# Kernel tuning notes

Measured on AMD Instinct MI355X. Metric: run time of the kernel, lower is better.

The kernel has to match this reference:

```python
import jax, jax.numpy as jnp
import numpy as np

B, S, D, T = 64, 512, 768, 9  # batch, seq_len, bert hidden, tag_size


def setup_inputs() -> dict:
    key = jax.random.key(0)
    ks = jax.random.split(key, 7)
    return {
        "embeds": jax.random.normal(ks[0], (B, S, D), jnp.float32),          # frozen BERT output
        "weight": jax.random.normal(ks[1], (T, D), jnp.float32) * 0.02,      # nn.Linear(768, tag_size)
        "bias": jnp.zeros((T,), jnp.float32),
        "start_transitions": jax.random.normal(ks[2], (T,), jnp.float32) * 0.1,
        "end_transitions": jax.random.normal(ks[3], (T,), jnp.float32) * 0.1,
        "transitions": jax.random.normal(ks[4], (T, T), jnp.float32) * 0.1,
        "tags": jax.random.randint(ks[5], (B, S), 0, T),
        "mask": jnp.ones((B, S), bool),  # torchcrf requires mask[:, 0] all on
    }


def reference(embeds, weight, bias, start_transitions, end_transitions, transitions, tags, mask):
    # Linear emission head (dropout is identity at eval)
    emissions = jnp.einsum("bsd,td->bst", embeds, weight) + bias  # [B,S,T]
    maskf = mask.astype(emissions.dtype)

    # --- numerator: score of gold path (torchcrf _compute_score) ---
    emit = jnp.take_along_axis(emissions, tags[:, :, None], axis=2)[:, :, 0]  # [B,S]
    trans = transitions[tags[:, :-1], tags[:, 1:]]                            # [B,S-1]
    num = start_transitions[tags[:, 0]] + emit[:, 0]
    num = num + jnp.sum((trans + emit[:, 1:]) * maskf[:, 1:], axis=1)
    seq_ends = jnp.sum(mask.astype(jnp.int32), axis=1) - 1                    # [B]
    last_tags = jnp.take_along_axis(tags, seq_ends[:, None], axis=1)[:, 0]
    num = num + end_transitions[last_tags]

    # --- denominator: forward algorithm (torchcrf _compute_normalizer) ---
    def step(score, xs):
        e_t, m_t = xs  # [B,T], [B]
        nxt = jax.nn.logsumexp(score[:, :, None] + transitions[None] + e_t[:, None, :], axis=1)
        return jnp.where(m_t[:, None], nxt, score), None

    score0 = start_transitions[None, :] + emissions[:, 0]                     # [B,T]
    xs = (jnp.swapaxes(emissions[:, 1:], 0, 1), jnp.swapaxes(mask[:, 1:], 0, 1))
    score, _ = jax.lax.scan(step, score0, xs)
    den = jax.nn.logsumexp(score + end_transitions[None, :], axis=1)          # [B]

    llh = num - den
    return -jnp.mean(llh)  # reduction='mean', negated
```

## Files before the change

### kernel.cpp

```cpp
#include <hip/hip_runtime.h>

#define BB 64
#define SS 512
#define DD 768
#define TT 9
#define CC 64
#define LL 8

template <int CTRL>
__device__ __forceinline__ float dpp_radd(float v) {
  return v + __int_as_float(__builtin_amdgcn_update_dpp(
                 0, __float_as_int(v), CTRL, 0xF, 0xF, true));
}
__device__ __forceinline__ float wave_sum_dpp(float v) {
  v = dpp_radd<0x111>(v);
  v = dpp_radd<0x112>(v);
  v = dpp_radd<0x114>(v);
  v = dpp_radd<0x118>(v);
  v = dpp_radd<0x142>(v);
  v = dpp_radd<0x143>(v);
  return v;
}

__global__ __launch_bounds__(256) void emis_kernel(
    const float* __restrict__ embeds, const float* __restrict__ weight,
    const float* __restrict__ bias, float* __restrict__ emis) {
  const int lane  = threadIdx.x & 63;
  const int wave  = blockIdx.x * (blockDim.x >> 6) + (threadIdx.x >> 6);
  const int nwav  = gridDim.x * (blockDim.x >> 6);

  float w[TT][12];
#pragma unroll
  for (int t = 0; t < TT; ++t) {
#pragma unroll
    for (int k = 0; k < 3; ++k) {
      const float4 v = *(const float4*)(weight + t * DD + k * 256 + lane * 4);
      w[t][k * 4 + 0] = v.x; w[t][k * 4 + 1] = v.y;
      w[t][k * 4 + 2] = v.z; w[t][k * 4 + 3] = v.w;
    }
  }
  float bb[TT];
#pragma unroll
  for (int t = 0; t < TT; ++t) bb[t] = bias[t];

  for (int row = wave; row < BB * SS; row += nwav) {
    const float* ep = embeds + (size_t)row * DD;
    float e[12];
#pragma unroll
    for (int k = 0; k < 3; ++k) {
      const float4 v = *(const float4*)(ep + k * 256 + lane * 4);
      e[k * 4 + 0] = v.x; e[k * 4 + 1] = v.y;
      e[k * 4 + 2] = v.z; e[k * 4 + 3] = v.w;
    }
    float acc[TT];
#pragma unroll
    for (int t = 0; t < TT; ++t) {
      float a = 0.f;
#pragma unroll
      for (int kk = 0; kk < 12; ++kk) a = fmaf(e[kk], w[t][kk], a);
      acc[t] = wave_sum_dpp(a);
    }
    if (lane == 63) {
#pragma unroll
      for (int t = 0; t < TT; ++t)
        emis[(size_t)row * TT + t] = acc[t] + bb[t];
    }
  }
}

__global__ __launch_bounds__(64) void crf_chunk_kernel(
    const float* __restrict__ emis, const float* __restrict__ trans,
    const float* __restrict__ startt, float* __restrict__ colM) {
  const int t = blockIdx.x * 64 + threadIdx.x;
  const int b = t / (CC * TT);
  const int r = t % (CC * TT);
  const int c = r / TT;
  const int j = r % TT;

  float et[TT][TT];
#pragma unroll
  for (int i = 0; i < TT; ++i)
#pragma unroll
    for (int k = 0; k < TT; ++k)
      et[i][k] = __expf(trans[i * TT + k]);

  float e[LL * TT];
  const float* eb = emis + (size_t)(b * SS + c * LL) * TT;
#pragma unroll
  for (int q = 0; q < (LL * TT) / 4; ++q) {
    const float4 v = *(const float4*)(eb + q * 4);
    e[q * 4 + 0] = v.x; e[q * 4 + 1] = v.y;
    e[q * 4 + 2] = v.z; e[q * 4 + 3] = v.w;
  }

  float v[TT];
#pragma unroll
  for (int i = 0; i < TT; ++i) v[i] = trans[i * TT + j] + e[(LL - 1) * TT + j];

#pragma unroll
  for (int ss = LL - 2; ss >= 0; --ss) {
    float w[TT];
#pragma unroll
    for (int k = 0; k < TT; ++k) w[k] = e[ss * TT + k] + v[k];
    if (ss == 0 && c == 0) {
#pragma unroll
      for (int k = 0; k < TT; ++k) w[k] += startt[k];
      float m = w[0];
#pragma unroll
      for (int k = 1; k < TT; ++k) m = fmaxf(m, w[k]);
      float sum = 0.f;
#pragma unroll
      for (int k = 0; k < TT; ++k) sum += __expf(w[k] - m);
      const float val = m + __logf(sum);
#pragma unroll
      for (int i = 0; i < TT; ++i) v[i] = val;
    } else {
      float m = w[0];
#pragma unroll
      for (int k = 1; k < TT; ++k) m = fmaxf(m, w[k]);
      float p[TT];
#pragma unroll
      for (int k = 0; k < TT; ++k) p[k] = __expf(w[k] - m);
#pragma unroll
      for (int i = 0; i < TT; ++i) {
        float sum = 0.f;
#pragma unroll
        for (int k = 0; k < TT; ++k) sum = fmaf(et[i][k], p[k], sum);
        v[i] = m + __logf(sum);
      }
    }
  }
  float* out = colM + ((size_t)(b * CC + c) * TT + j) * TT;
#pragma unroll
  for (int i = 0; i < TT; ++i) out[i] = v[i];
}

__global__ __launch_bounds__(576) void crf_combine_kernel(
    const float* __restrict__ colM, const float* __restrict__ emis,
    const float* __restrict__ trans, const float* __restrict__ startt,
    const float* __restrict__ endt, const int* __restrict__ tags,
    float* __restrict__ partial) {
  const int b   = blockIdx.x;
  const int tid = threadIdx.x;
  __shared__ float A[CC * 81];
  __shared__ float Bm[(CC / 2) * 81];
  __shared__ float red2[16];

  const float4* src4 = (const float4*)(colM + (size_t)b * CC * 81);
  float4* A4 = (float4*)A;
  for (int q = tid; q < (CC * 81) / 4; q += 576) A4[q] = src4[q];

  const float* E  = emis + (size_t)b * SS * TT;
  const int*   tg = tags + (size_t)b * SS;
  float nsum = 0.f;
  if (tid < SS) {
    const int tt = tg[tid];
    nsum = E[tid * TT + tt];
    nsum += (tid == 0) ? startt[tt] : trans[tg[tid - 1] * TT + tt];
  }
  nsum = wave_sum_dpp(nsum);
  if ((tid & 63) == 63) red2[tid >> 6] = nsum;
  __syncthreads();

  float* srcb = A;
  float* dstb = Bm;
  for (int n = CC / 2; n >= 1; n >>= 1) {
    const int tasks = n * TT;
    if (tid < tasks) {
      const int p = tid / TT, j = tid % TT;
      float a[81], wv[TT];
      const float* AT = srcb + (2 * p) * 81;
      const float* BT = srcb + (2 * p + 1) * 81;
#pragma unroll
      for (int q = 0; q < 81; ++q) a[q] = AT[q];
#pragma unroll
      for (int k = 0; k < TT; ++k) wv[k] = BT[j * TT + k];
      float* OT = dstb + p * 81;
#pragma unroll
      for (int i = 0; i < TT; ++i) {
        float x[TT];
#pragma unroll
        for (int k = 0; k < TT; ++k) x[k] = a[k * TT + i] + wv[k];
        float m = x[0];
#pragma unroll
        for (int k = 1; k < TT; ++k) m = fmaxf(m, x[k]);
        float sum = 0.f;
#pragma unroll
        for (int k = 0; k < TT; ++k) sum += __expf(x[k] - m);
        OT[j * TT + i] = m + __logf(sum);
      }
    }
    __syncthreads();
    float* tmp = srcb; srcb = dstb; dstb = tmp;
  }
  if (tid == 0) {
    float num = red2[0];
#pragma unroll
    for (int wv = 1; wv < 9; ++wv) num += red2[wv];
    num += endt[tg[SS - 1]];
    float x[TT];
#pragma unroll
    for (int j = 0; j < TT; ++j) x[j] = srcb[j * TT + 0] + endt[j];
    float m = x[0];
#pragma unroll
    for (int j = 1; j < TT; ++j) m = fmaxf(m, x[j]);
    float sum = 0.f;
#pragma unroll
    for (int j = 0; j < TT; ++j) sum += __expf(x[j] - m);
    partial[b] = (m + __logf(sum)) - num;
  }
}

__global__ __launch_bounds__(64) void crf_kernel(
    const float* __restrict__ emis, const float* __restrict__ trans,
    const float* __restrict__ startt, const float* __restrict__ endt,
    const int* __restrict__ tags, float* __restrict__ partial) {
  const int b    = blockIdx.x;
  const int lane = threadIdx.x;
  const float* E = emis + (size_t)b * SS * TT;
  const int*  tg = tags + (size_t)b * SS;

  float nsum = 0.f;
  for (int s = lane; s < SS; s += 64) {
    const int t  = tg[s];
    const float ev = E[s * TT + t];
    if (s == 0) nsum += startt[t] + ev;
    else        nsum += trans[tg[s - 1] * TT + t] + ev;
  }
#pragma unroll
  for (int off = 32; off > 0; off >>= 1) nsum += __shfl_xor(nsum, off, 64);
  const float num = nsum + endt[tg[SS - 1]];

  const int j = (lane < TT) ? lane : (TT - 1);
  float tc[TT];
#pragma unroll
  for (int i = 0; i < TT; ++i) tc[i] = trans[i * TT + j];

  float sc = startt[j] + E[j];
  for (int s = 1; s < SS; ++s) {
    float x[TT];
#pragma unroll
    for (int i = 0; i < TT; ++i) x[i] = __shfl(sc, i, 64) + tc[i];
    float m = x[0];
#pragma unroll
    for (int i = 1; i < TT; ++i) m = fmaxf(m, x[i]);
    float ssum = 0.f;
#pragma unroll
    for (int i = 0; i < TT; ++i) ssum += __expf(x[i] - m);
    sc = m + __logf(ssum) + E[s * TT + j];
  }
  const float v = sc + endt[j];
  float y[TT];
#pragma unroll
  for (int i = 0; i < TT; ++i) y[i] = __shfl(v, i, 64);
  float m = y[0];
#pragma unroll
  for (int i = 1; i < TT; ++i) m = fmaxf(m, y[i]);
  float ssum = 0.f;
#pragma unroll
  for (int i = 0; i < TT; ++i) ssum += __expf(y[i] - m);
  if (lane == 0) partial[b] = (m + __logf(ssum)) - num;
}

__global__ __launch_bounds__(64) void reduce_kernel(
    const float* __restrict__ partial, float* __restrict__ out) {
  float v = partial[threadIdx.x];
#pragma unroll
  for (int off = 32; off > 0; off >>= 1) v += __shfl_xor(v, off, 64);
  if (threadIdx.x == 0) out[0] = v * (1.0f / BB);
}

extern "C" void kernel_launch(void* const* d_in, const int* in_sizes, int n_in,
                              void* d_out, int out_size, void* d_ws, size_t ws_size,
                              hipStream_t stream) {
  const float* embeds = (const float*)d_in[0];
  const float* weight = (const float*)d_in[1];
  const float* bias   = (const float*)d_in[2];
  const float* startt = (const float*)d_in[3];
  const float* endt   = (const float*)d_in[4];
  const float* trans  = (const float*)d_in[5];
  const int*   tags   = (const int*)d_in[6];

  float* ws      = (float*)d_ws;
  float* emis    = ws;
  float* colM    = ws + (size_t)BB * SS * TT;
  float* partial = colM + (size_t)BB * CC * 81;
  float* out     = (float*)d_out;

  const size_t need = ((size_t)BB * SS * TT + (size_t)BB * CC * 81 + BB) * 4;

  emis_kernel<<<2048, 256, 0, stream>>>(embeds, weight, bias, emis);
  if (ws_size >= need) {
    crf_chunk_kernel<<<(BB * CC * TT) / 64, 64, 0, stream>>>(emis, trans, startt, colM);
    crf_combine_kernel<<<BB, 576, 0, stream>>>(colM, emis, trans, startt, endt, tags, partial);
  } else {
    partial = ws + (size_t)BB * SS * TT;
    crf_kernel<<<BB, 64, 0, stream>>>(emis, trans, startt, endt, tags, partial);
  }
  reduce_kernel<<<1, 64, 0, stream>>>(partial, out);
}
```

Before: 47.25 us.

## Fuse emission GEMV with CRF chunk stage and fold final reduction into combine

Merges the emission projection, the per-chunk CRF log-semiring transfer matrices and the gold-path numerator partials into one kernel that keeps emissions in shared memory, so the emission array never goes to global memory. The final mean reduction moves into the combine kernel through an atomic counter with a last-block pattern, which removes the separate reduce launch. This cuts four launches to two and removes a global round trip. In exchange the fused kernel uses a fixed grid of 512 blocks with 8 rows per wave, drops the small-workspace fallback path, and resets the counter inside the first kernel.

```diff
diff --git a/kernel.cpp b/kernel.cpp
--- a/kernel.cpp
+++ b/kernel.cpp
@@ -6,6 +6,7 @@
 #define TT 9
 #define CC 64
 #define LL 8
+#define EMSTRIDE 76
 
 template <int CTRL>
 __device__ __forceinline__ float dpp_radd(float v) {
@@ -22,29 +23,47 @@
   return v;
 }
 
-__global__ __launch_bounds__(256) void emis_kernel(
+__global__ __launch_bounds__(512) void k1_fused(
     const float* __restrict__ embeds, const float* __restrict__ weight,
-    const float* __restrict__ bias, float* __restrict__ emis) {
-  const int lane  = threadIdx.x & 63;
-  const int wave  = blockIdx.x * (blockDim.x >> 6) + (threadIdx.x >> 6);
-  const int nwav  = gridDim.x * (blockDim.x >> 6);
-
-  float w[TT][12];
+    const float* __restrict__ bias, const float* __restrict__ startt,
+    const float* __restrict__ trans, const int* __restrict__ tags,
+    float* __restrict__ colM, float* __restrict__ numpart,
+    int* __restrict__ ctr) {
+  const int tid  = threadIdx.x;
+  const int lane = tid & 63;
+  const int wv   = tid >> 6;
+  const int b    = blockIdx.x >> 3;
+  const int cg   = blockIdx.x & 7;
+
+  if (blockIdx.x == 0 && tid == 0) ctr[0] = 0;
+
+  __shared__ float em[8 * EMSTRIDE];
+  __shared__ float trl[81];
+  __shared__ float etl[81];
+  if (tid < 81) {
+    const float tv = trans[tid];
+    trl[tid] = tv;
+    etl[tid] = __expf(tv);
+  }
+
+  float wreg[TT][12];
 #pragma unroll
   for (int t = 0; t < TT; ++t) {
 #pragma unroll
     for (int k = 0; k < 3; ++k) {
       const float4 v = *(const float4*)(weight + t * DD + k * 256 + lane * 4);
-      w[t][k * 4 + 0] = v.x; w[t][k * 4 + 1] = v.y;
-      w[t][k * 4 + 2] = v.z; w[t][k * 4 + 3] = v.w;
+      wreg[t][k * 4 + 0] = v.x; wreg[t][k * 4 + 1] = v.y;
+      wreg[t][k * 4 + 2] = v.z; wreg[t][k * 4 + 3] = v.w;
     }
   }
   float bb[TT];
 #pragma unroll
   for (int t = 0; t < TT; ++t) bb[t] = bias[t];
 
-  for (int row = wave; row < BB * SS; row += nwav) {
-    const float* ep = embeds + (size_t)row * DD;
+  const int row0 = b * SS + cg * 64 + wv * 8;
+#pragma unroll
+  for (int r = 0; r < LL; ++r) {
+    const float* ep = embeds + (size_t)(row0 + r) * DD;
     float e[12];
 #pragma unroll
     for (int k = 0; k < 3; ++k) {
@@ -57,116 +76,95 @@
     for (int t = 0; t < TT; ++t) {
       float a = 0.f;
 #pragma unroll
-      for (int kk = 0; kk < 12; ++kk) a = fmaf(e[kk], w[t][kk], a);
+      for (int kk = 0; kk < 12; ++kk) a = fmaf(e[kk], wreg[t][kk], a);
       acc[t] = wave_sum_dpp(a);
     }
     if (lane == 63) {
 #pragma unroll
       for (int t = 0; t < TT; ++t)
-        emis[(size_t)row * TT + t] = acc[t] + bb[t];
-    }
-  }
-}
-
-__global__ __launch_bounds__(64) void crf_chunk_kernel(
-    const float* __restrict__ emis, const float* __restrict__ trans,
-    const float* __restrict__ startt, float* __restrict__ colM) {
-  const int t = blockIdx.x * 64 + threadIdx.x;
-  const int b = t / (CC * TT);
-  const int r = t % (CC * TT);
-  const int c = r / TT;
-  const int j = r % TT;
-
-  float et[TT][TT];
-#pragma unroll
-  for (int i = 0; i < TT; ++i)
-#pragma unroll
-    for (int k = 0; k < TT; ++k)
-      et[i][k] = __expf(trans[i * TT + k]);
-
-  float e[LL * TT];
-  const float* eb = emis + (size_t)(b * SS + c * LL) * TT;
-#pragma unroll
-  for (int q = 0; q < (LL * TT) / 4; ++q) {
-    const float4 v = *(const float4*)(eb + q * 4);
-    e[q * 4 + 0] = v.x; e[q * 4 + 1] = v.y;
-    e[q * 4 + 2] = v.z; e[q * 4 + 3] = v.w;
-  }
-
-  float v[TT];
-#pragma unroll
-  for (int i = 0; i < TT; ++i) v[i] = trans[i * TT + j] + e[(LL - 1) * TT + j];
-
-#pragma unroll
-  for (int ss = LL - 2; ss >= 0; --ss) {
-    float w[TT];
-#pragma unroll
-    for (int k = 0; k < TT; ++k) w[k] = e[ss * TT + k] + v[k];
-    if (ss == 0 && c == 0) {
-#pragma unroll
-      for (int k = 0; k < TT; ++k) w[k] += startt[k];
-      float m = w[0];
-#pragma unroll
-      for (int k = 1; k < TT; ++k) m = fmaxf(m, w[k]);
-      float sum = 0.f;
-#pragma unroll
-      for (int k = 0; k < TT; ++k) sum += __expf(w[k] - m);
-      const float val = m + __logf(sum);
-#pragma unroll
-      for (int i = 0; i < TT; ++i) v[i] = val;
-    } else {
-      float m = w[0];
-#pragma unroll
-      for (int k = 1; k < TT; ++k) m = fmaxf(m, w[k]);
-      float p[TT];
-#pragma unroll
-      for (int k = 0; k < TT; ++k) p[k] = __expf(w[k] - m);
-#pragma unroll
-      for (int i = 0; i < TT; ++i) {
+        em[wv * EMSTRIDE + r * TT + t] = acc[t] + bb[t];
+    }
+  }
+  __syncthreads();
+
+  if (wv == 2) {
+    const int sl = lane;
+    const int s  = cg * 64 + sl;
+    const int* tg = tags + (size_t)b * SS;
+    const int tt = tg[s];
+    float nterm = em[(sl >> 3) * EMSTRIDE + (sl & 7) * TT + tt];
+    nterm += (s == 0) ? startt[tt] : trl[tg[s - 1] * TT + tt];
+    nterm = wave_sum_dpp(nterm);
+    if (lane == 63) numpart[b * 8 + cg] = nterm;
+  }
+
+  if (tid < 8 * TT) {
+    const int cl = tid / TT, j = tid % TT;
+    const int gc = cg * 8 + cl;
+    const float* e = em + cl * EMSTRIDE;
+
+    float v[TT];
+#pragma unroll
+    for (int i = 0; i < TT; ++i) v[i] = trl[i * TT + j] + e[(LL - 1) * TT + j];
+
+#pragma unroll
+    for (int ss = LL - 2; ss >= 0; --ss) {
+      float x[TT];
+#pragma unroll
+      for (int k = 0; k < TT; ++k) x[k] = e[ss * TT + k] + v[k];
+      if (ss == 0 && gc == 0) {
+#pragma unroll
+        for (int k = 0; k < TT; ++k) x[k] += startt[k];
+        float m = x[0];
+#pragma unroll
+        for (int k = 1; k < TT; ++k) m = fmaxf(m, x[k]);
         float sum = 0.f;
 #pragma unroll
-        for (int k = 0; k < TT; ++k) sum = fmaf(et[i][k], p[k], sum);
-        v[i] = m + __logf(sum);
+        for (int k = 0; k < TT; ++k) sum += __expf(x[k] - m);
+        const float val = m + __logf(sum);
+#pragma unroll
+        for (int i = 0; i < TT; ++i) v[i] = val;
+      } else {
+        float m = x[0];
+#pragma unroll
+        for (int k = 1; k < TT; ++k) m = fmaxf(m, x[k]);
+        float p[TT];
+#pragma unroll
+        for (int k = 0; k < TT; ++k) p[k] = __expf(x[k] - m);
+#pragma unroll
+        for (int i = 0; i < TT; ++i) {
+          float sum = 0.f;
+#pragma unroll
+          for (int k = 0; k < TT; ++k) sum = fmaf(etl[i * TT + k], p[k], sum);
+          v[i] = m + __logf(sum);
+        }
       }
     }
-  }
-  float* out = colM + ((size_t)(b * CC + c) * TT + j) * TT;
-#pragma unroll
-  for (int i = 0; i < TT; ++i) out[i] = v[i];
-}
-
-__global__ __launch_bounds__(576) void crf_combine_kernel(
-    const float* __restrict__ colM, const float* __restrict__ emis,
-    const float* __restrict__ trans, const float* __restrict__ startt,
+    float* out = colM + ((size_t)(b * CC + gc) * TT + j) * TT;
+#pragma unroll
+    for (int i = 0; i < TT; ++i) out[i] = v[i];
+  }
+}
+
+__global__ __launch_bounds__(576) void k2_combine_fin(
+    const float* __restrict__ colM, const float* __restrict__ numpart,
     const float* __restrict__ endt, const int* __restrict__ tags,
-    float* __restrict__ partial) {
+    float* __restrict__ partial, int* __restrict__ ctr,
+    float* __restrict__ out) {
   const int b   = blockIdx.x;
   const int tid = threadIdx.x;
   __shared__ float A[CC * 81];
   __shared__ float Bm[(CC / 2) * 81];
-  __shared__ float red2[16];
 
   const float4* src4 = (const float4*)(colM + (size_t)b * CC * 81);
   float4* A4 = (float4*)A;
   for (int q = tid; q < (CC * 81) / 4; q += 576) A4[q] = src4[q];
-
-  const float* E  = emis + (size_t)b * SS * TT;
-  const int*   tg = tags + (size_t)b * SS;
-  float nsum = 0.f;
-  if (tid < SS) {
-    const int tt = tg[tid];
-    nsum = E[tid * TT + tt];
-    nsum += (tid == 0) ? startt[tt] : trans[tg[tid - 1] * TT + tt];
-  }
-  nsum = wave_sum_dpp(nsum);
-  if ((tid & 63) == 63) red2[tid >> 6] = nsum;
   __syncthreads();
 
   float* srcb = A;
   float* dstb = Bm;
   for (int n = CC / 2; n >= 1; n >>= 1) {
-    const int tasks = n * TT;
-    if (tid < tasks) {
+    if (tid < n * TT) {
       const int p = tid / TT, j = tid % TT;
       float a[81], wv[TT];
       const float* AT = srcb + (2 * p) * 81;
@@ -193,11 +191,14 @@
     __syncthreads();
     float* tmp = srcb; srcb = dstb; dstb = tmp;
   }
+
   if (tid == 0) {
-    float num = red2[0];
-#pragma unroll
-    for (int wv = 1; wv < 9; ++wv) num += red2[wv];
+    const int* tg = tags + (size_t)b * SS;
+    float num = 0.f;
+#pragma unroll
+    for (int q = 0; q < 8; ++q) num += numpart[b * 8 + q];
     num += endt[tg[SS - 1]];
+
     float x[TT];
 #pragma unroll
     for (int j = 0; j < TT; ++j) x[j] = srcb[j * TT + 0] + endt[j];
@@ -208,66 +209,18 @@
 #pragma unroll
     for (int j = 0; j < TT; ++j) sum += __expf(x[j] - m);
     partial[b] = (m + __logf(sum)) - num;
-  }
-}
-
-__global__ __launch_bounds__(64) void crf_kernel(
-    const float* __restrict__ emis, const float* __restrict__ trans,
-    const float* __restrict__ startt, const float* __restrict__ endt,
-    const int* __restrict__ tags, float* __restrict__ partial) {
-  const int b    = blockIdx.x;
-  const int lane = threadIdx.x;
-  const float* E = emis + (size_t)b * SS * TT;
-  const int*  tg = tags + (size_t)b * SS;
-
-  float nsum = 0.f;
-  for (int s = lane; s < SS; s += 64) {
-    const int t  = tg[s];
-    const float ev = E[s * TT + t];
-    if (s == 0) nsum += startt[t] + ev;
-    else        nsum += trans[tg[s - 1] * TT + t] + ev;
-  }
-#pragma unroll
-  for (int off = 32; off > 0; off >>= 1) nsum += __shfl_xor(nsum, off, 64);
-  const float num = nsum + endt[tg[SS - 1]];
-
-  const int j = (lane < TT) ? lane : (TT - 1);
-  float tc[TT];
-#pragma unroll
-  for (int i = 0; i < TT; ++i) tc[i] = trans[i * TT + j];
-
-  float sc = startt[j] + E[j];
-  for (int s = 1; s < SS; ++s) {
-    float x[TT];
-#pragma unroll
-    for (int i = 0; i < TT; ++i) x[i] = __shfl(sc, i, 64) + tc[i];
-    float m = x[0];
-#pragma unroll
-    for (int i = 1; i < TT; ++i) m = fmaxf(m, x[i]);
-    float ssum = 0.f;
-#pragma unroll
-    for (int i = 0; i < TT; ++i) ssum += __expf(x[i] - m);
-    sc = m + __logf(ssum) + E[s * TT + j];
-  }
-  const float v = sc + endt[j];
-  float y[TT];
-#pragma unroll
-  for (int i = 0; i < TT; ++i) y[i] = __shfl(v, i, 64);
-  float m = y[0];
-#pragma unroll
-  for (int i = 1; i < TT; ++i) m = fmaxf(m, y[i]);
-  float ssum = 0.f;
-#pragma unroll
-  for (int i = 0; i < TT; ++i) ssum += __expf(y[i] - m);
-  if (lane == 0) partial[b] = (m + __logf(ssum)) - num;
-}
-
-__global__ __launch_bounds__(64) void reduce_kernel(
-    const float* __restrict__ partial, float* __restrict__ out) {
-  float v = partial[threadIdx.x];
-#pragma unroll
-  for (int off = 32; off > 0; off >>= 1) v += __shfl_xor(v, off, 64);
-  if (threadIdx.x == 0) out[0] = v * (1.0f / BB);
+
+    __threadfence();
+    const int old = atomicAdd(ctr, 1);
+    if (old == BB - 1) {
+      __threadfence();
+      volatile const float* vp = partial;
+      float s = 0.f;
+#pragma unroll
+      for (int i = 0; i < BB; ++i) s += vp[i];
+      out[0] = s * (1.0f / BB);
+    }
+  }
 }
 
 extern "C" void kernel_launch(void* const* d_in, const int* in_sizes, int n_in,
@@ -282,20 +235,14 @@
   const int*   tags   = (const int*)d_in[6];
 
   float* ws      = (float*)d_ws;
-  float* emis    = ws;
-  float* colM    = ws + (size_t)BB * SS * TT;
-  float* partial = colM + (size_t)BB * CC * 81;
+  float* colM    = ws;
+  float* numpart = colM + (size_t)BB * CC * 81;
+  float* partial = numpart + BB * 8;
+  int*   ctr     = (int*)(partial + BB);
   float* out     = (float*)d_out;
 
-  const size_t need = ((size_t)BB * SS * TT + (size_t)BB * CC * 81 + BB) * 4;
-
-  emis_kernel<<<2048, 256, 0, stream>>>(embeds, weight, bias, emis);
-  if (ws_size >= need) {
-    crf_chunk_kernel<<<(BB * CC * TT) / 64, 64, 0, stream>>>(emis, trans, startt, colM);
-    crf_combine_kernel<<<BB, 576, 0, stream>>>(colM, emis, trans, startt, endt, tags, partial);
-  } else {
-    partial = ws + (size_t)BB * SS * TT;
-    crf_kernel<<<BB, 64, 0, stream>>>(emis, trans, startt, endt, tags, partial);
-  }
-  reduce_kernel<<<1, 64, 0, stream>>>(partial, out);
-}
+  k1_fused<<<BB * 8, 512, 0, stream>>>(embeds, weight, bias, startt, trans,
+                                       tags, colM, numpart, ctr);
+  k2_combine_fin<<<BB, 576, 0, stream>>>(colM, numpart, endt, tags, partial,
+                                         ctr, out);
+}
```

After: 48.97 us. 1.04x slower.
